# Kernel tuning notes

Hardware: AMD Instinct MI355X
Metric: run time of the kernel (lower is better)

The kernel has to match this reference:

```python
import jax, jax.numpy as jnp
import numpy as np

D_IN, H1, H2, N_CLS, BATCH = 1024, 2048, 2048, 1000, 8192


def setup_inputs() -> dict:
    key = jax.random.key(0)
    ks = jax.random.split(key, 7)
    x = jax.random.normal(ks[0], (BATCH, D_IN), dtype=jnp.float32)
    # torch.nn.Linear default init scale ~ 1/sqrt(fan_in); weights stored [out, in]
    W1 = jax.random.normal(ks[1], (H1, D_IN), dtype=jnp.float32) / np.sqrt(D_IN).astype(np.float32)
    b1 = jax.random.normal(ks[2], (H1,), dtype=jnp.float32) * 0.01
    W2 = jax.random.normal(ks[3], (H2, H1), dtype=jnp.float32) / np.sqrt(H1).astype(np.float32)
    b2 = jax.random.normal(ks[4], (H2,), dtype=jnp.float32) * 0.01
    W3 = jax.random.normal(ks[5], (N_CLS, H2), dtype=jnp.float32) / np.sqrt(H2).astype(np.float32)
    b3 = jax.random.normal(ks[6], (N_CLS,), dtype=jnp.float32) * 0.01
    return {"x": x, "W1": W1, "b1": b1, "W2": W2, "b2": b2, "W3": W3, "b3": b3}


def reference(x, W1, b1, W2, b2, W3, b3):
    # forward_with_coactivations: classifier = [Linear, ReLU, Linear, ReLU, Linear]
    # activation points: the two ReLU layers and the final Linear.
    prev_act = (x > 0).astype(jnp.float32)  # [B, D_IN]

    z1 = x @ W1.T + b1                      # [B, H1]
    a1 = jax.nn.relu(z1)
    act1 = (z1 > 0).astype(jnp.float32)     # (relu(z)>0) == (z>0)
    # sum_s outer(prev_act[s], act1[s]) == prev_act.T @ act1
    coact0 = jnp.einsum('bi,bj->ij', prev_act, act1)  # [D_IN, H1]

    z2 = a1 @ W2.T + b2                     # [B, H2]
    a2 = jax.nn.relu(z2)
    act2 = (z2 > 0).astype(jnp.float32)
    coact1 = jnp.einsum('bi,bj->ij', act1, act2)      # [H1, H2]

    logits = a2 @ W3.T + b3                 # [B, N_CLS]
    act3 = (logits > 0).astype(jnp.float32)
    coact2 = jnp.einsum('bi,bj->ij', act2, act3)      # [H2, N_CLS]

    return logits, coact0, coact1, coact2
```

## Files before the change

### kernel.cpp

```cpp
#include <hip/hip_runtime.h>
#include <hip/hip_bf16.h>


typedef short v8s __attribute__((ext_vector_type(8)));
typedef float v4f __attribute__((ext_vector_type(4)));
typedef int v4i __attribute__((ext_vector_type(4)));

enum { MODE_RELU = 0, MODE_LOGITS = 1 };

__device__ __forceinline__ void async_cp16(const void* gsrc, void* ldst) {
  __builtin_amdgcn_global_load_lds(
      (const __attribute__((address_space(1))) void*)gsrc,
      (__attribute__((address_space(3))) void*)ldst, 16, 0, 0);
}

#define FENCE asm volatile("" ::: "memory")
#define BAR()                         \
  do {                                \
    FENCE;                            \
    __builtin_amdgcn_s_barrier();     \
    FENCE;                            \
  } while (0)
#define WAITL()                                          \
  do {                                                   \
    asm volatile("s_waitcnt lgkmcnt(0)" ::: "memory");   \
    __builtin_amdgcn_sched_barrier(0);                   \
  } while (0)
#define WAITV(n)                                           \
  do {                                                     \
    asm volatile("s_waitcnt vmcnt(" #n ")" ::: "memory");  \
    __builtin_amdgcn_sched_barrier(0);                     \
  } while (0)
#define PRIO1 __builtin_amdgcn_s_setprio(1)
#define PRIO0 __builtin_amdgcn_s_setprio(0)

__global__ __launch_bounds__(512, 2) void gemm256_relu_wt(
    const __hip_bfloat16* __restrict__ A, const __hip_bfloat16* __restrict__ B,
    const float* __restrict__ bias, __hip_bfloat16* __restrict__ Cout,
    char* __restrict__ Tout, int K, int ldc) {
  __shared__ char smem[131072];
  const int t = threadIdx.x;
  const int m0 = blockIdx.y * 256;
  const int n0 = blockIdx.x * 256;

  const int c0 = t, c1 = 512 + t;
  const int r0s = c0 >> 3, r1s = c1 >> 3;
  const int goff0 = r0s * K + ((c0 & 7) ^ (r0s & 7)) * 8;
  const int goff1 = r1s * K + ((c1 & 7) ^ (r1s & 7)) * 8;
  const int loff0 = c0 * 16, loff1 = c1 * 16;

  const __hip_bfloat16* const Abase = A + (size_t)m0 * K;
  const __hip_bfloat16* const Bbase = B + (size_t)n0 * K;
  const size_t hk = (size_t)128 * K;

  char* const pA0l = smem;
  char* const pA0h = smem + 16384;
  char* const pB0l = smem + 32768;
  char* const pB0h = smem + 49152;
  char* const pA1l = smem + 65536;
  char* const pA1h = smem + 81920;
  char* const pB1l = smem + 98304;
  char* const pB1h = smem + 114688;

  const int lane = t & 63;
  const int wave = t >> 6;
  const int wm = wave >> 2;
  const int wn = wave & 3;
  const int lrow = lane & 15;
  const int quad = lane >> 4;
  const int sl0 = ((quad ^ (lrow & 7)) * 16);
  const int sl1 = (((quad + 4) ^ (lrow & 7)) * 16);
  const int ardA = (wm * 128 + lrow) * 128;
  const int ardB = (wn * 64 + lrow) * 128;

  v4f acc[8][4] = {};
  v8s alo[4][2], ahi[4][2], blo[2][2], bhi[2][2];

#define STAGE(dst, src)                                          \
  do {                                                           \
    async_cp16((const void*)((src) + goff0), (void*)((dst) + loff0)); \
    async_cp16((const void*)((src) + goff1), (void*)((dst) + loff1)); \
  } while (0)

#define LDA_H(dst, hh, bb)                                                   \
  _Pragma("unroll") for (int mi = 0; mi < 4; mi++) {                         \
    dst[mi][0] =                                                             \
        *(const v8s*)(smem + (bb) + ardA + (hh)*8192 + mi * 2048 + sl0);     \
    dst[mi][1] =                                                             \
        *(const v8s*)(smem + (bb) + ardA + (hh)*8192 + mi * 2048 + sl1);     \
  }

#define LDB_P(dst, pp, bb)                                                    \
  _Pragma("unroll") for (int ni = 0; ni < 2; ni++) {                          \
    dst[ni][0] = *(const v8s*)(smem + (bb) + 32768 + ardB +                   \
                               ((pp)*2 + ni) * 2048 + sl0);                   \
    dst[ni][1] = *(const v8s*)(smem + (bb) + 32768 + ardB +                   \
                               ((pp)*2 + ni) * 2048 + sl1);                   \
  }

#define MMA_Q(af, bf, MB, NB)                                               \
  _Pragma("unroll") for (int mi = 0; mi < 4; mi++)                          \
      _Pragma("unroll") for (int ni = 0; ni < 2; ni++)                      \
          _Pragma("unroll") for (int ks = 0; ks < 2; ks++)                  \
              acc[(MB) + mi][(NB) + ni] =                                   \
      __builtin_amdgcn_mfma_f32_16x16x32_bf16(                              \
          af[mi][ks], bf[ni][ks], acc[(MB) + mi][(NB) + ni], 0, 0, 0);

  STAGE(pA0l, Abase);
  STAGE(pA0h, Abase + hk);
  STAGE(pB0l, Bbase);
  STAGE(pB0h, Bbase + hk);
  STAGE(pA1l, Abase + 64);
  STAGE(pA1h, Abase + hk + 64);
  WAITV(4);
  BAR();

  const int NI = K >> 7;
#pragma unroll 1
  for (int i = 0; i < NI - 1; ++i) {
    const int k1 = (2 * i + 1) << 6;
    const int k2 = (2 * i + 2) << 6;
    const int k3 = (2 * i + 3) << 6;
    LDA_H(alo, 0, 0);
    LDB_P(blo, 0, 0);
    STAGE(pB1l, Bbase + k1);
    BAR();
    WAITL();
    PRIO1; MMA_Q(alo, blo, 0, 0); PRIO0;
    BAR();
    LDA_H(ahi, 1, 0);
    STAGE(pB1h, Bbase + hk + k1);
    BAR();
    WAITL();
    PRIO1; MMA_Q(ahi, blo, 4, 0); PRIO0;
    BAR();
    LDB_P(bhi, 1, 0);
    STAGE(pA0l, Abase + k2);
    BAR();
    WAITL();
    PRIO1; MMA_Q(alo, bhi, 0, 2); PRIO0;
    BAR();
    STAGE(pA0h, Abase + hk + k2);
    BAR();
    PRIO1; MMA_Q(ahi, bhi, 4, 2); PRIO0;
    WAITV(4);
    BAR();
    LDA_H(alo, 0, 65536);
    LDB_P(blo, 0, 65536);
    STAGE(pB0l, Bbase + k2);
    BAR();
    WAITL();
    PRIO1; MMA_Q(alo, blo, 0, 0); PRIO0;
    BAR();
    LDA_H(ahi, 1, 65536);
    STAGE(pB0h, Bbase + hk + k2);
    BAR();
    WAITL();
    PRIO1; MMA_Q(ahi, blo, 4, 0); PRIO0;
    BAR();
    LDB_P(bhi, 1, 65536);
    STAGE(pA1l, Abase + k3);
    BAR();
    WAITL();
    PRIO1; MMA_Q(alo, bhi, 0, 2); PRIO0;
    BAR();
    STAGE(pA1h, Abase + hk + k3);
    BAR();
    PRIO1; MMA_Q(ahi, bhi, 4, 2); PRIO0;
    WAITV(4);
    BAR();
  }
  {
    const int k1 = (2 * (NI - 1) + 1) << 6;
    LDA_H(alo, 0, 0);
    LDB_P(blo, 0, 0);
    STAGE(pB1l, Bbase + k1);
    BAR();
    WAITL();
    PRIO1; MMA_Q(alo, blo, 0, 0); PRIO0;
    BAR();
    LDA_H(ahi, 1, 0);
    STAGE(pB1h, Bbase + hk + k1);
    BAR();
    WAITL();
    PRIO1; MMA_Q(ahi, blo, 4, 0); PRIO0;
    BAR();
    LDB_P(bhi, 1, 0);
    BAR();
    WAITL();
    PRIO1; MMA_Q(alo, bhi, 0, 2); PRIO0;
    BAR();
    BAR();
    PRIO1; MMA_Q(ahi, bhi, 4, 2); PRIO0;
    WAITV(0);
    BAR();
    LDA_H(alo, 0, 65536);
    LDB_P(blo, 0, 65536);
    BAR();
    WAITL();
    PRIO1; MMA_Q(alo, blo, 0, 0); PRIO0;
    BAR();
    LDA_H(ahi, 1, 65536);
    BAR();
    WAITL();
    PRIO1; MMA_Q(ahi, blo, 4, 0); PRIO0;
    BAR();
    LDB_P(bhi, 1, 65536);
    BAR();
    WAITL();
    PRIO1; MMA_Q(alo, bhi, 0, 2); PRIO0;
    BAR();
    BAR();
    PRIO1; MMA_Q(ahi, bhi, 4, 2); PRIO0;
    BAR();
  }
#undef STAGE
#undef LDA_H
#undef LDB_P
#undef MMA_Q

  float bv[4];
#pragma unroll
  for (int ni = 0; ni < 4; ni++) bv[ni] = bias[n0 + wn * 64 + ni * 16 + lrow];

#pragma unroll
  for (int mi = 0; mi < 8; mi++) {
    const int rowb = m0 + wm * 128 + mi * 16 + quad * 4;
#pragma unroll
    for (int ni = 0; ni < 4; ni++) {
      const int col = n0 + wn * 64 + ni * 16 + lrow;
#pragma unroll
      for (int r = 0; r < 4; r++) {
        const float v = acc[mi][ni][r] + bv[ni];
        Cout[(size_t)(rowb + r) * ldc + col] =
            __float2bfloat16(v > 0.f ? v : 0.f);
      }
    }
  }

  char* const sT = smem;
#pragma unroll
  for (int ni = 0; ni < 4; ni++) {
    const int c = wn * 64 + ni * 16 + lrow;
#pragma unroll
    for (int mi = 0; mi < 8; mi++) {
      const int rw = wm * 128 + mi * 16 + quad * 4;
      char4 bits;
      bits.x = (acc[mi][ni][0] + bv[ni] > 0.f) ? 1 : 0;
      bits.y = (acc[mi][ni][1] + bv[ni] > 0.f) ? 1 : 0;
      bits.z = (acc[mi][ni][2] + bv[ni] > 0.f) ? 1 : 0;
      bits.w = (acc[mi][ni][3] + bv[ni] > 0.f) ? 1 : 0;
      *(char4*)&sT[c * 272 + rw] = bits;
    }
  }
  __syncthreads();
  const int rw2 = t >> 1;
  const int hf = (t & 1) * 128;
  char* dst = Tout + (size_t)(n0 + rw2) * 8192 + m0 + hf;
  const char* src = sT + rw2 * 272 + hf;
#pragma unroll
  for (int j = 0; j < 8; j++)
    *(int4*)(dst + j * 16) = *(const int4*)(src + j * 16);
}

template <int MODE, int WT>
__global__ __launch_bounds__(256) void gemm_nt(
    const __hip_bfloat16* __restrict__ A, const __hip_bfloat16* __restrict__ B,
    const float* __restrict__ bias, void* __restrict__ Cout,
    char* __restrict__ Tout, int M, int N, int K, int n_store, int ldc) {
  __shared__ char smem[32768];
  __hip_bfloat16* sA = (__hip_bfloat16*)smem;
  __hip_bfloat16* sB = (__hip_bfloat16*)(smem + 16384);
  const int t = threadIdx.x;
  const int m0 = blockIdx.y * 128;
  const int n0 = blockIdx.x * 128;

  const __hip_bfloat16* aG[4];
  const __hip_bfloat16* bG[4];
  char* lA[4];
  char* lB[4];
#pragma unroll
  for (int j = 0; j < 4; j++) {
    const int c = j * 256 + t;
    const int row = c >> 3;
    const int g = (c & 7) ^ (row & 7);
    aG[j] = A + (size_t)(m0 + row) * K + g * 8;
    bG[j] = B + (size_t)(n0 + row) * K + g * 8;
    lA[j] = (char*)sA + c * 16;
    lB[j] = (char*)sB + c * 16;
  }

  const int lane = t & 63;
  const int wave = t >> 6;
  const int wm = (wave & 1) * 64;
  const int wn = (wave >> 1) * 64;
  const int lrow = lane & 15;
  const int quad = lane >> 4;

  const int g0 = quad ^ (lrow & 7);
  const __hip_bfloat16* pa0 = sA + (wm + lrow) * 64 + g0 * 8;
  const __hip_bfloat16* pa1 = sA + (wm + lrow) * 64 + (g0 ^ 4) * 8;
  const __hip_bfloat16* pb0 = sB + (wn + lrow) * 64 + g0 * 8;
  const __hip_bfloat16* pb1 = sB + (wn + lrow) * 64 + (g0 ^ 4) * 8;

  v4f acc[4][4] = {};

  for (int k0 = 0; k0 < K; k0 += 64) {
#pragma unroll
    for (int j = 0; j < 4; j++) {
      async_cp16(aG[j] + k0, lA[j]);
      async_cp16(bG[j] + k0, lB[j]);
    }
    __syncthreads();

    v8s a0[4], b0[4], a1[4], b1[4];
#pragma unroll
    for (int i = 0; i < 4; i++) {
      a0[i] = *(const v8s*)(pa0 + i * 16 * 64);
      b0[i] = *(const v8s*)(pb0 + i * 16 * 64);
    }
#pragma unroll
    for (int mi = 0; mi < 4; mi++)
#pragma unroll
      for (int ni = 0; ni < 4; ni++)
        acc[mi][ni] = __builtin_amdgcn_mfma_f32_16x16x32_bf16(
            a0[mi], b0[ni], acc[mi][ni], 0, 0, 0);
#pragma unroll
    for (int i = 0; i < 4; i++) {
      a1[i] = *(const v8s*)(pa1 + i * 16 * 64);
      b1[i] = *(const v8s*)(pb1 + i * 16 * 64);
    }
#pragma unroll
    for (int mi = 0; mi < 4; mi++)
#pragma unroll
      for (int ni = 0; ni < 4; ni++)
        acc[mi][ni] = __builtin_amdgcn_mfma_f32_16x16x32_bf16(
            a1[mi], b1[ni], acc[mi][ni], 0, 0, 0);
    __syncthreads();
  }

  float bvv[4];
#pragma unroll
  for (int ni = 0; ni < 4; ni++) {
    const int col = n0 + wn + ni * 16 + lrow;
    bvv[ni] = 0.f;
    if (MODE == MODE_RELU) bvv[ni] = bias[col];
    else if (col < n_store) bvv[ni] = bias[col];
  }

#pragma unroll
  for (int ni = 0; ni < 4; ni++) {
    const int col = n0 + wn + ni * 16 + lrow;
#pragma unroll
    for (int mi = 0; mi < 4; mi++) {
      const int rowb = m0 + wm + mi * 16 + quad * 4;
#pragma unroll
      for (int r = 0; r < 4; r++) {
        const int row = rowb + r;
        const float v = acc[mi][ni][r] + bvv[ni];
        if (MODE == MODE_RELU) {
          ((__hip_bfloat16*)Cout)[(size_t)row * ldc + col] =
              __float2bfloat16(v > 0.f ? v : 0.f);
        } else {
          if (col < n_store)
            ((float*)Cout)[(size_t)row * ldc + col] = v;
        }
      }
    }
  }

  if (WT) {
    char* sT = smem;
#pragma unroll
    for (int ni = 0; ni < 4; ni++) {
      const int c = wn + ni * 16 + lrow;
#pragma unroll
      for (int mi = 0; mi < 4; mi++) {
        const int r = wm + mi * 16 + quad * 4;
        char4 bits;
        bits.x = (acc[mi][ni][0] + bvv[ni] > 0.f) ? 1 : 0;
        bits.y = (acc[mi][ni][1] + bvv[ni] > 0.f) ? 1 : 0;
        bits.z = (acc[mi][ni][2] + bvv[ni] > 0.f) ? 1 : 0;
        bits.w = (acc[mi][ni][3] + bvv[ni] > 0.f) ? 1 : 0;
        *(char4*)&sT[c * 144 + r] = bits;
      }
    }
    __syncthreads();
    const int c2 = t >> 1;
    const int hf = (t & 1) * 64;
    char* dst = Tout + (size_t)(n0 + c2) * 8192 + m0 + hf;
    const char* src = sT + c2 * 144 + hf;
#pragma unroll
    for (int j = 0; j < 4; j++)
      *(int4*)(dst + j * 16) = *(const int4*)(src + j * 16);
  }
}

__global__ __launch_bounds__(256) void gemm_nt_i8(
    const char* __restrict__ A, const char* __restrict__ B,
    float* __restrict__ P, int M, int N, int Kc, int n_store, size_t slice) {
  __shared__ char sA[128 * 128];
  __shared__ char sB[128 * 128];
  const int t = threadIdx.x;
  const int m0 = blockIdx.y * 128;
  const int n0 = blockIdx.x * 128;
  const int kbeg = blockIdx.z * Kc;
  const int kend = kbeg + Kc;
  const size_t K = (size_t)Kc * gridDim.z;
  float* __restrict__ Pz = P + (size_t)blockIdx.z * slice;

  const char* aG[4];
  const char* bG[4];
  char* lA[4];
  char* lB[4];
#pragma unroll
  for (int j = 0; j < 4; j++) {
    const int c = j * 256 + t;
    const int row = c >> 3;
    const int g = (c & 7) ^ (row & 7);
    aG[j] = A + (size_t)(m0 + row) * K + g * 16;
    bG[j] = B + (size_t)(n0 + row) * K + g * 16;
    lA[j] = sA + c * 16;
    lB[j] = sB + c * 16;
  }

  const int lane = t & 63;
  const int wave = t >> 6;
  const int wm = (wave & 1) * 64;
  const int wn = (wave >> 1) * 64;
  const int lrow = lane & 15;
  const int quad = lane >> 4;

  const int g0 = quad ^ (lrow & 7);
  const char* pa0 = sA + (wm + lrow) * 128 + g0 * 16;
  const char* pa1 = sA + (wm + lrow) * 128 + (g0 ^ 4) * 16;
  const char* pb0 = sB + (wn + lrow) * 128 + g0 * 16;
  const char* pb1 = sB + (wn + lrow) * 128 + (g0 ^ 4) * 16;

  v4i acc[4][4] = {};

  for (int k0 = kbeg; k0 < kend; k0 += 128) {
#pragma unroll
    for (int j = 0; j < 4; j++) {
      async_cp16(aG[j] + k0, lA[j]);
      async_cp16(bG[j] + k0, lB[j]);
    }
    __syncthreads();

    v4i a0[4], b0[4], a1[4], b1[4];
#pragma unroll
    for (int i = 0; i < 4; i++) {
      a0[i] = *(const v4i*)(pa0 + i * 16 * 128);
      b0[i] = *(const v4i*)(pb0 + i * 16 * 128);
    }
#pragma unroll
    for (int mi = 0; mi < 4; mi++)
#pragma unroll
      for (int ni = 0; ni < 4; ni++)
        acc[mi][ni] = __builtin_amdgcn_mfma_i32_16x16x64_i8(
            a0[mi], b0[ni], acc[mi][ni], 0, 0, 0);
#pragma unroll
    for (int i = 0; i < 4; i++) {
      a1[i] = *(const v4i*)(pa1 + i * 16 * 128);
      b1[i] = *(const v4i*)(pb1 + i * 16 * 128);
    }
#pragma unroll
    for (int mi = 0; mi < 4; mi++)
#pragma unroll
      for (int ni = 0; ni < 4; ni++)
        acc[mi][ni] = __builtin_amdgcn_mfma_i32_16x16x64_i8(
            a1[mi], b1[ni], acc[mi][ni], 0, 0, 0);
    __syncthreads();
  }

#pragma unroll
  for (int ni = 0; ni < 4; ni++) {
    const int col = n0 + wn + ni * 16 + lrow;
    if (col >= n_store) continue;
#pragma unroll
    for (int mi = 0; mi < 4; mi++) {
      const int rowb = m0 + wm + mi * 16 + quad * 4;
#pragma unroll
      for (int r = 0; r < 4; r++) {
        Pz[(size_t)(rowb + r) * n_store + col] = (float)acc[mi][ni][r];
      }
    }
  }
}

template <int Z>
__global__ __launch_bounds__(256) void reduce_part(
    const float* __restrict__ P, float* __restrict__ out, int n4, size_t slice) {
  const int i = blockIdx.x * 256 + threadIdx.x;
  if (i >= n4) return;
  float4 s = ((const float4*)P)[i];
#pragma unroll
  for (int z = 1; z < Z; z++) {
    const float4 v = ((const float4*)(P + (size_t)z * slice))[i];
    s.x += v.x; s.y += v.y; s.z += v.z; s.w += v.w;
  }
  ((float4*)out)[i] = s;
}

__global__ __launch_bounds__(256) void transpose_bin8f(
    const float* __restrict__ in, char* __restrict__ out,
    int R, int ldin, int Cphys) {
  __shared__ char tile[64][65];
  const int c0 = blockIdx.x * 64;
  const int r0 = blockIdx.y * 64;
  const int tx = threadIdx.x & 63;
  const int ty = threadIdx.x >> 6;
#pragma unroll
  for (int i = 0; i < 64; i += 4) {
    const int c = c0 + tx;
    const int r = r0 + ty + i;
    float v = 0.f;
    if (c < Cphys) v = in[(size_t)r * ldin + c];
    tile[ty + i][tx] = (v > 0.f) ? 1 : 0;
  }
  __syncthreads();
  const int u = threadIdx.x & 15;
  const int cg = threadIdx.x >> 4;
#pragma unroll
  for (int i = 0; i < 64; i += 16) {
    const int col = cg + i;
    char4 v;
    v.x = tile[4 * u + 0][col];
    v.y = tile[4 * u + 1][col];
    v.z = tile[4 * u + 2][col];
    v.w = tile[4 * u + 3][col];
    *(char4*)&out[(size_t)(c0 + col) * R + r0 + 4 * u] = v;
  }
}

struct Cvt4 {
  const float* src[4];
  __hip_bfloat16* dst[4];
  int n4[4];
};
__global__ __launch_bounds__(256) void f32_to_bf16_multi(Cvt4 c) {
  int i = blockIdx.x * 256 + threadIdx.x;
#pragma unroll
  for (int s = 0; s < 4; s++) {
    if (i < c.n4[s]) {
      const float4 v = ((const float4*)c.src[s])[i];
      union { __hip_bfloat16 h[4]; ushort4 u; } cv;
      cv.h[0] = __float2bfloat16(v.x);
      cv.h[1] = __float2bfloat16(v.y);
      cv.h[2] = __float2bfloat16(v.z);
      cv.h[3] = __float2bfloat16(v.w);
      ((ushort4*)c.dst[s])[i] = cv.u;
      return;
    }
    i -= c.n4[s];
  }
}

extern "C" void kernel_launch(void* const* d_in, const int* in_sizes, int n_in,
                              void* d_out, int out_size, void* d_ws, size_t ws_size,
                              hipStream_t stream) {
  const float* x  = (const float*)d_in[0];
  const float* W1 = (const float*)d_in[1];
  const float* b1 = (const float*)d_in[2];
  const float* W2 = (const float*)d_in[3];
  const float* b2 = (const float*)d_in[4];
  const float* W3 = (const float*)d_in[5];
  const float* b3 = (const float*)d_in[6];

  float* logits = (float*)d_out;
  float* coact0 = logits + (size_t)8192 * 1000;
  float* coact1 = coact0 + (size_t)1024 * 2048;
  float* coact2 = coact1 + (size_t)2048 * 2048;

  char* ws = (char*)d_ws;
  size_t off = 0;
  auto alloc = [&](size_t bytes) {
    char* p = ws + off;
    off += (bytes + 255) & ~(size_t)255;
    return p;
  };
  __hip_bfloat16* X   = (__hip_bfloat16*)alloc((size_t)8192 * 1024 * 2);
  __hip_bfloat16* W1b = (__hip_bfloat16*)alloc((size_t)2048 * 1024 * 2);
  __hip_bfloat16* W2b = (__hip_bfloat16*)alloc((size_t)2048 * 2048 * 2);
  __hip_bfloat16* W3b = (__hip_bfloat16*)alloc((size_t)1024 * 2048 * 2);
  __hip_bfloat16* A1  = (__hip_bfloat16*)alloc((size_t)8192 * 2048 * 2);
  __hip_bfloat16* A2  = (__hip_bfloat16*)alloc((size_t)8192 * 2048 * 2);
  char* T0 = (char*)alloc((size_t)1024 * 8192);
  char* T1 = (char*)alloc((size_t)2048 * 8192);
  char* T2 = (char*)X;
  char* T3 = (char*)W2b;
  float* P = (float*)A1;

  const dim3 blk(256);

  {
    Cvt4 c;
    c.src[0] = x;  c.dst[0] = X;   c.n4[0] = 8192 * 1024 / 4;
    c.src[1] = W1; c.dst[1] = W1b; c.n4[1] = 2048 * 1024 / 4;
    c.src[2] = W2; c.dst[2] = W2b; c.n4[2] = 2048 * 2048 / 4;
    c.src[3] = W3; c.dst[3] = W3b; c.n4[3] = 1000 * 2048 / 4;
    const int total = c.n4[0] + c.n4[1] + c.n4[2] + c.n4[3];
    f32_to_bf16_multi<<<(total + 255) / 256, blk, 0, stream>>>(c);
  }

  transpose_bin8f<<<dim3(16, 128), blk, 0, stream>>>(x, T0, 8192, 1024, 1024);

  gemm256_relu_wt<<<dim3(8, 32), dim3(512), 0, stream>>>(
      X, W1b, b1, A1, T1, 1024, 2048);

  gemm256_relu_wt<<<dim3(8, 32), dim3(512), 0, stream>>>(
      A1, W2b, b2, A2, T2, 2048, 2048);

  gemm_nt<MODE_LOGITS, 1><<<dim3(8, 64), blk, 0, stream>>>(
      A2, W3b, b3, logits, T3, 8192, 1024, 2048, 1000, 1000);

  gemm_nt_i8<<<dim3(16, 8, 4), blk, 0, stream>>>(T0, T1, P,
                                                 1024, 2048, 2048, 2048,
                                                 (size_t)1024 * 2048);
  reduce_part<4><<<1024 * 2048 / 4 / 256, blk, 0, stream>>>(
      P, coact0, 1024 * 2048 / 4, (size_t)1024 * 2048);

  gemm_nt_i8<<<dim3(16, 16, 2), blk, 0, stream>>>(T1, T2, P,
                                                  2048, 2048, 4096, 2048,
                                                  (size_t)2048 * 2048);
  reduce_part<2><<<2048 * 2048 / 4 / 256, blk, 0, stream>>>(
      P, coact1, 2048 * 2048 / 4, (size_t)2048 * 2048);

  gemm_nt_i8<<<dim3(8, 16, 4), blk, 0, stream>>>(T2, T3, P,
                                                 2048, 1024, 2048, 1000,
                                                 (size_t)2048 * 1000);
  reduce_part<4><<<2048 * 1000 / 4 / 256, blk, 0, stream>>>(
      P, coact2, 2048 * 1000 / 4, (size_t)2048 * 1000);
}
```

Before: 429.4 us.

## Software-pipeline LDS fragment loads across MMA quadrants and swizzle block order for L2 locality

Restructures the GEMM main loop so the last MMA quadrant of each half-step is deferred into the next stage. LDS fragment reads for the next quadrants are issued earlier, with partial lgkmcnt waits, so they overlap with the MFMAs. The A-tile global stages are paired together, which removes several barriers per iteration. It also remaps block IDs into 8 interleaved chunks, which is meant to improve L2 or XCD locality. In exchange it adds a peeled prologue and needs more live registers, which could cause spilling or occupancy issues; the remap assumes the block count divides by 8.

```diff
diff --git a/kernel.cpp b/kernel.cpp
--- a/kernel.cpp
+++ b/kernel.cpp
@@ -26,11 +26,17 @@
     asm volatile("s_waitcnt lgkmcnt(0)" ::: "memory");   \
     __builtin_amdgcn_sched_barrier(0);                   \
   } while (0)
+#define WAITLN(n)                                          \
+  do {                                                     \
+    asm volatile("s_waitcnt lgkmcnt(" #n ")" ::: "memory"); \
+    __builtin_amdgcn_sched_barrier(0);                     \
+  } while (0)
 #define WAITV(n)                                           \
   do {                                                     \
     asm volatile("s_waitcnt vmcnt(" #n ")" ::: "memory");  \
     __builtin_amdgcn_sched_barrier(0);                     \
   } while (0)
+#define SCHEDB __builtin_amdgcn_sched_barrier(0)
 #define PRIO1 __builtin_amdgcn_s_setprio(1)
 #define PRIO0 __builtin_amdgcn_s_setprio(0)
 
@@ -40,8 +46,11 @@
     char* __restrict__ Tout, int K, int ldc) {
   __shared__ char smem[131072];
   const int t = threadIdx.x;
-  const int m0 = blockIdx.y * 256;
-  const int n0 = blockIdx.x * 256;
+  const int f = blockIdx.y * gridDim.x + blockIdx.x;
+  const int cpx = (gridDim.x * gridDim.y) >> 3;
+  const int w = (f & 7) * cpx + (f >> 3);
+  const int m0 = (w / gridDim.x) * 256;
+  const int n0 = (w % gridDim.x) * 256;
 
   const int c0 = t, c1 = 512 + t;
   const int r0s = c0 >> 3, r1s = c1 >> 3;
@@ -76,8 +85,8 @@
   v4f acc[8][4] = {};
   v8s alo[4][2], ahi[4][2], blo[2][2], bhi[2][2];
 
-#define STAGE(dst, src)                                          \
-  do {                                                           \
+#define STAGE(dst, src)                                               \
+  do {                                                                \
     async_cp16((const void*)((src) + goff0), (void*)((dst) + loff0)); \
     async_cp16((const void*)((src) + goff1), (void*)((dst) + loff1)); \
   } while (0)
@@ -116,103 +125,144 @@
   BAR();
 
   const int NI = K >> 7;
+
+  LDA_H(alo, 0, 0);
+  LDB_P(blo, 0, 0);
+  STAGE(pB1l, Bbase + 64);
+  BAR();
+  LDA_H(ahi, 1, 0);
+  LDB_P(bhi, 1, 0);
+  STAGE(pB1h, Bbase + hk + 64);
+  BAR();
+  WAITLN(12);
+  PRIO1; MMA_Q(alo, blo, 0, 0); PRIO0;
+  BAR();
+  WAITL();
+  PRIO1; MMA_Q(ahi, blo, 4, 0); PRIO0;
+  BAR();
+  SCHEDB;
+  STAGE(pA0l, Abase + 128);
+  STAGE(pA0h, Abase + hk + 128);
+  SCHEDB;
+  PRIO1; MMA_Q(alo, bhi, 0, 2); PRIO0;
+  WAITV(4);
+  BAR();
+  LDA_H(alo, 0, 65536);
+  LDB_P(blo, 0, 65536);
+  STAGE(pB0l, Bbase + 128);
+  BAR();
+  PRIO1; MMA_Q(ahi, bhi, 4, 2); PRIO0;
+  BAR();
+  LDA_H(ahi, 1, 65536);
+  LDB_P(bhi, 1, 65536);
+  STAGE(pB0h, Bbase + hk + 128);
+  BAR();
+  WAITLN(12);
+  PRIO1; MMA_Q(alo, blo, 0, 0); PRIO0;
+  BAR();
+  WAITL();
+  PRIO1; MMA_Q(ahi, blo, 4, 0); PRIO0;
+  BAR();
+  SCHEDB;
+  STAGE(pA1l, Abase + 192);
+  STAGE(pA1h, Abase + hk + 192);
+  SCHEDB;
+  PRIO1; MMA_Q(alo, bhi, 0, 2); PRIO0;
+  WAITV(4);
+  BAR();
+
 #pragma unroll 1
-  for (int i = 0; i < NI - 1; ++i) {
-    const int k1 = (2 * i + 1) << 6;
-    const int k2 = (2 * i + 2) << 6;
-    const int k3 = (2 * i + 3) << 6;
+  for (int i = 1; i <= NI - 2; ++i) {
+    const __hip_bfloat16* Bo = Bbase + (2 * i + 1) * 64;
+    const __hip_bfloat16* Ae2 = Abase + (2 * i + 2) * 64;
+    const __hip_bfloat16* Be2 = Bbase + (2 * i + 2) * 64;
+    const __hip_bfloat16* Ao2 = Abase + (2 * i + 3) * 64;
     LDA_H(alo, 0, 0);
     LDB_P(blo, 0, 0);
-    STAGE(pB1l, Bbase + k1);
-    BAR();
-    WAITL();
+    STAGE(pB1l, Bo);
+    BAR();
+    PRIO1; MMA_Q(ahi, bhi, 4, 2); PRIO0;
+    BAR();
+    LDA_H(ahi, 1, 0);
+    LDB_P(bhi, 1, 0);
+    STAGE(pB1h, Bo + hk);
+    BAR();
+    WAITLN(12);
     PRIO1; MMA_Q(alo, blo, 0, 0); PRIO0;
-    BAR();
-    LDA_H(ahi, 1, 0);
-    STAGE(pB1h, Bbase + hk + k1);
     BAR();
     WAITL();
     PRIO1; MMA_Q(ahi, blo, 4, 0); PRIO0;
     BAR();
-    LDB_P(bhi, 1, 0);
-    STAGE(pA0l, Abase + k2);
-    BAR();
-    WAITL();
+    SCHEDB;
+    STAGE(pA0l, Ae2);
+    STAGE(pA0h, Ae2 + hk);
+    SCHEDB;
     PRIO1; MMA_Q(alo, bhi, 0, 2); PRIO0;
-    BAR();
-    STAGE(pA0h, Abase + hk + k2);
-    BAR();
-    PRIO1; MMA_Q(ahi, bhi, 4, 2); PRIO0;
     WAITV(4);
     BAR();
     LDA_H(alo, 0, 65536);
     LDB_P(blo, 0, 65536);
-    STAGE(pB0l, Bbase + k2);
-    BAR();
-    WAITL();
+    STAGE(pB0l, Be2);
+    BAR();
+    PRIO1; MMA_Q(ahi, bhi, 4, 2); PRIO0;
+    BAR();
+    LDA_H(ahi, 1, 65536);
+    LDB_P(bhi, 1, 65536);
+    STAGE(pB0h, Be2 + hk);
+    BAR();
+    WAITLN(12);
     PRIO1; MMA_Q(alo, blo, 0, 0); PRIO0;
-    BAR();
-    LDA_H(ahi, 1, 65536);
-    STAGE(pB0h, Bbase + hk + k2);
     BAR();
     WAITL();
     PRIO1; MMA_Q(ahi, blo, 4, 0); PRIO0;
     BAR();
-    LDB_P(bhi, 1, 65536);
-    STAGE(pA1l, Abase + k3);
-    BAR();
-    WAITL();
+    SCHEDB;
+    STAGE(pA1l, Ao2);
+    STAGE(pA1h, Ao2 + hk);
+    SCHEDB;
     PRIO1; MMA_Q(alo, bhi, 0, 2); PRIO0;
-    BAR();
-    STAGE(pA1h, Abase + hk + k3);
-    BAR();
-    PRIO1; MMA_Q(ahi, bhi, 4, 2); PRIO0;
     WAITV(4);
     BAR();
   }
+
   {
-    const int k1 = (2 * (NI - 1) + 1) << 6;
+    const __hip_bfloat16* Bo = Bbase + (size_t)(K - 64);
     LDA_H(alo, 0, 0);
     LDB_P(blo, 0, 0);
-    STAGE(pB1l, Bbase + k1);
-    BAR();
-    WAITL();
+    STAGE(pB1l, Bo);
+    BAR();
+    PRIO1; MMA_Q(ahi, bhi, 4, 2); PRIO0;
+    BAR();
+    LDA_H(ahi, 1, 0);
+    LDB_P(bhi, 1, 0);
+    STAGE(pB1h, Bo + hk);
+    BAR();
+    WAITLN(12);
     PRIO1; MMA_Q(alo, blo, 0, 0); PRIO0;
-    BAR();
-    LDA_H(ahi, 1, 0);
-    STAGE(pB1h, Bbase + hk + k1);
     BAR();
     WAITL();
     PRIO1; MMA_Q(ahi, blo, 4, 0); PRIO0;
     BAR();
-    LDB_P(bhi, 1, 0);
-    BAR();
-    WAITL();
     PRIO1; MMA_Q(alo, bhi, 0, 2); PRIO0;
-    BAR();
-    BAR();
-    PRIO1; MMA_Q(ahi, bhi, 4, 2); PRIO0;
     WAITV(0);
     BAR();
     LDA_H(alo, 0, 65536);
     LDB_P(blo, 0, 65536);
     BAR();
-    WAITL();
+    PRIO1; MMA_Q(ahi, bhi, 4, 2); PRIO0;
+    BAR();
+    LDA_H(ahi, 1, 65536);
+    LDB_P(bhi, 1, 65536);
+    BAR();
+    WAITLN(12);
     PRIO1; MMA_Q(alo, blo, 0, 0); PRIO0;
-    BAR();
-    LDA_H(ahi, 1, 65536);
     BAR();
     WAITL();
     PRIO1; MMA_Q(ahi, blo, 4, 0); PRIO0;
     BAR();
-    LDB_P(bhi, 1, 65536);
-    BAR();
-    WAITL();
     PRIO1; MMA_Q(alo, bhi, 0, 2); PRIO0;
     BAR();
-    BAR();
     PRIO1; MMA_Q(ahi, bhi, 4, 2); PRIO0;
-    BAR();
   }
 #undef STAGE
 #undef LDA_H
```

Measured after the change: 507.0 us. 18.1% more time.

## Restructure GEMM main loop pipeline with finer-grained vmcnt waits and rotated MMA

Applied to the files above, without the earlier changes.

Reworks the double-buffered GEMM main loop. The fourth MMA quadrant of each half-iteration is rotated into the next phase, so every MMA step is now preceded by an LDS read and an async global-to-LDS stage. Waits use per-stage vmcnt counts instead of one coarse wait per half-iteration. The separate epilogue iteration is folded into the loop by wrapping the prefetch indices to tile 0, which issues redundant dummy loads at the end. The aim is to keep more global loads in flight and remove idle stalls between MFMA bursts, at the cost of extra loads and more complex wait accounting that could hide ordering bugs.

```diff
diff --git a/kernel.cpp b/kernel.cpp
--- a/kernel.cpp
+++ b/kernel.cpp
@@ -76,8 +76,8 @@
   v4f acc[8][4] = {};
   v8s alo[4][2], ahi[4][2], blo[2][2], bhi[2][2];
 
-#define STAGE(dst, src)                                          \
-  do {                                                           \
+#define STAGE(dst, src)                                               \
+  do {                                                                \
     async_cp16((const void*)((src) + goff0), (void*)((dst) + loff0)); \
     async_cp16((const void*)((src) + goff1), (void*)((dst) + loff1)); \
   } while (0)
@@ -111,109 +111,82 @@
   STAGE(pB0l, Bbase);
   STAGE(pB0h, Bbase + hk);
   STAGE(pA1l, Abase + 64);
-  STAGE(pA1h, Abase + hk + 64);
-  WAITV(4);
+  WAITV(8);
   BAR();
 
   const int NI = K >> 7;
+  const int NT = K >> 6;
+
 #pragma unroll 1
-  for (int i = 0; i < NI - 1; ++i) {
-    const int k1 = (2 * i + 1) << 6;
-    const int k2 = (2 * i + 2) << 6;
-    const int k3 = (2 * i + 3) << 6;
+  for (int i = 0; i < NI; ++i) {
+    const int to = 2 * i + 1;
+    const int t2 = (2 * i + 2 < NT) ? 2 * i + 2 : 0;
+    const int t3 = (2 * i + 3 < NT) ? 2 * i + 3 : 0;
+    const __hip_bfloat16* Ao = Abase + to * 64;
+    const __hip_bfloat16* Bo = Bbase + to * 64;
+    const __hip_bfloat16* A2 = Abase + t2 * 64;
+    const __hip_bfloat16* B2 = Bbase + t2 * 64;
+    const __hip_bfloat16* A3 = Abase + t3 * 64;
     LDA_H(alo, 0, 0);
+    STAGE(pA1h, Ao + hk);
+    WAITV(6);
+    BAR();
+    WAITL();
+    if (i) { PRIO1; MMA_Q(ahi, bhi, 4, 2); PRIO0; }
+    BAR();
     LDB_P(blo, 0, 0);
-    STAGE(pB1l, Bbase + k1);
+    STAGE(pB1l, Bo);
+    WAITV(10);
     BAR();
     WAITL();
     PRIO1; MMA_Q(alo, blo, 0, 0); PRIO0;
     BAR();
     LDA_H(ahi, 1, 0);
-    STAGE(pB1h, Bbase + hk + k1);
+    STAGE(pB1h, Bo + hk);
+    WAITV(8);
     BAR();
     WAITL();
     PRIO1; MMA_Q(ahi, blo, 4, 0); PRIO0;
     BAR();
     LDB_P(bhi, 1, 0);
-    STAGE(pA0l, Abase + k2);
+    STAGE(pA0l, A2);
+    WAITV(8);
     BAR();
     WAITL();
     PRIO1; MMA_Q(alo, bhi, 0, 2); PRIO0;
     BAR();
-    STAGE(pA0h, Abase + hk + k2);
-    BAR();
+    LDA_H(alo, 0, 65536);
+    STAGE(pA0h, A2 + hk);
+    WAITV(6);
+    BAR();
+    WAITL();
     PRIO1; MMA_Q(ahi, bhi, 4, 2); PRIO0;
-    WAITV(4);
-    BAR();
-    LDA_H(alo, 0, 65536);
+    BAR();
     LDB_P(blo, 0, 65536);
-    STAGE(pB0l, Bbase + k2);
+    STAGE(pB0l, B2);
+    WAITV(10);
     BAR();
     WAITL();
     PRIO1; MMA_Q(alo, blo, 0, 0); PRIO0;
     BAR();
     LDA_H(ahi, 1, 65536);
-    STAGE(pB0h, Bbase + hk + k2);
+    STAGE(pB0h, B2 + hk);
+    WAITV(8);
     BAR();
     WAITL();
     PRIO1; MMA_Q(ahi, blo, 4, 0); PRIO0;
     BAR();
     LDB_P(bhi, 1, 65536);
-    STAGE(pA1l, Abase + k3);
+    STAGE(pA1l, A3);
+    WAITV(8);
     BAR();
     WAITL();
     PRIO1; MMA_Q(alo, bhi, 0, 2); PRIO0;
     BAR();
-    STAGE(pA1h, Abase + hk + k3);
-    BAR();
-    PRIO1; MMA_Q(ahi, bhi, 4, 2); PRIO0;
-    WAITV(4);
-    BAR();
-  }
-  {
-    const int k1 = (2 * (NI - 1) + 1) << 6;
-    LDA_H(alo, 0, 0);
-    LDB_P(blo, 0, 0);
-    STAGE(pB1l, Bbase + k1);
-    BAR();
-    WAITL();
-    PRIO1; MMA_Q(alo, blo, 0, 0); PRIO0;
-    BAR();
-    LDA_H(ahi, 1, 0);
-    STAGE(pB1h, Bbase + hk + k1);
-    BAR();
-    WAITL();
-    PRIO1; MMA_Q(ahi, blo, 4, 0); PRIO0;
-    BAR();
-    LDB_P(bhi, 1, 0);
-    BAR();
-    WAITL();
-    PRIO1; MMA_Q(alo, bhi, 0, 2); PRIO0;
-    BAR();
-    BAR();
-    PRIO1; MMA_Q(ahi, bhi, 4, 2); PRIO0;
-    WAITV(0);
-    BAR();
-    LDA_H(alo, 0, 65536);
-    LDB_P(blo, 0, 65536);
-    BAR();
-    WAITL();
-    PRIO1; MMA_Q(alo, blo, 0, 0); PRIO0;
-    BAR();
-    LDA_H(ahi, 1, 65536);
-    BAR();
-    WAITL();
-    PRIO1; MMA_Q(ahi, blo, 4, 0); PRIO0;
-    BAR();
-    LDB_P(bhi, 1, 65536);
-    BAR();
-    WAITL();
-    PRIO1; MMA_Q(alo, bhi, 0, 2); PRIO0;
-    BAR();
-    BAR();
-    PRIO1; MMA_Q(ahi, bhi, 4, 2); PRIO0;
-    BAR();
-  }
+  }
+  PRIO1; MMA_Q(ahi, bhi, 4, 2); PRIO0;
+  WAITV(0);
+  BAR();
 #undef STAGE
 #undef LDA_H
 #undef LDB_P
```

Measured after the change: 421.4 us. Within noise of the previous version (-1.9%).
